# Optimization experiments

Hardware: AMD Instinct MI355X
Metric: run time of the kernel (lower is better)

Reference implementation:

```python
import jax, jax.numpy as jnp
import numpy as np

THRESHOLD = 0.5

def setup_inputs() -> dict:
    key = jax.random.key(0)
    ks = jax.random.split(key, 7)
    dim, hidden = 1024, 4096
    x = jax.random.normal(ks[0], (4, 4096, dim), dtype=jnp.float32)
    # router: Linear(dim, 1)
    W_r = jax.random.normal(ks[1], (dim, 1), dtype=jnp.float32) / np.sqrt(dim)
    b_r = jnp.zeros((1,), dtype=jnp.float32)
    # MLP: Linear(dim, hidden) -> ReLU -> Linear(hidden, dim)
    W1 = jax.random.normal(ks[2], (dim, hidden), dtype=jnp.float32) / np.sqrt(dim)
    b1 = jnp.zeros((hidden,), dtype=jnp.float32)
    W2 = jax.random.normal(ks[3], (hidden, dim), dtype=jnp.float32) / np.sqrt(hidden)
    b2 = jnp.zeros((dim,), dtype=jnp.float32)
    return {"x": x, "W_r": W_r, "b_r": b_r, "W1": W1, "b1": b1, "W2": W2, "b2": b2}

def reference(x, W_r, b_r, W1, b1, W2, b2):
    # router logits per token: [B, S]
    logits = (jnp.einsum('bsd,do->bso', x, W_r) + b_r)[..., 0]
    probs = jax.nn.sigmoid(logits)
    mask = probs > THRESHOLD  # [B, S] bool
    # dense equivalent of gather-MLP-scatter: compute MLP everywhere, select per token
    h = jax.nn.relu(jnp.einsum('bsd,dh->bsh', x, W1) + b1)
    processed = jnp.einsum('bsh,hd->bsd', h, W2) + b2
    output = jnp.where(mask[..., None], processed, x)
    frac = jnp.mean(mask.astype(jnp.float32))
    return (output, frac)
```

## Files before the change

### kernel.cpp

```cpp
#include <hip/hip_runtime.h>
#include <hip/hip_bf16.h>

#define TOKENS 16384
#define DIM 1024
#define HID 4096

typedef __attribute__((ext_vector_type(8))) short short8;
typedef __attribute__((ext_vector_type(4))) float f32x4;

__device__ __forceinline__ unsigned short f2bf(float f) {
  union { float f; unsigned int u; } v; v.f = f;
  unsigned int r = v.u + 0x7fffu + ((v.u >> 16) & 1u);
  return (unsigned short)(r >> 16);
}

__device__ __forceinline__ void async16(const void* g, void* lds) {
  __builtin_amdgcn_global_load_lds((const __attribute__((address_space(1))) void*)g,
                                   (__attribute__((address_space(3))) void*)lds, 16, 0, 0);
}

__global__ __launch_bounds__(256) void router_kernel(
    const float* __restrict__ x, const float* __restrict__ Wr, const float* __restrict__ br,
    float* __restrict__ out, unsigned short* __restrict__ xb,
    int* __restrict__ idx, int* __restrict__ counter)
{
  __shared__ unsigned char selLds[16];
  int wid = threadIdx.x >> 6, lane = threadIdx.x & 63;
  const float4* wr4 = (const float4*)Wr;
  float4 w[4];
#pragma unroll
  for (int j = 0; j < 4; ++j) w[j] = wr4[lane + 64 * j];
  float b0 = br[0];

#pragma unroll
  for (int t = 0; t < 4; ++t) {
    int token = blockIdx.x * 16 + wid * 4 + t;
    const float4* xr = (const float4*)(x + (size_t)token * DIM);
    float4 v[4];
#pragma unroll
    for (int j = 0; j < 4; ++j) v[j] = xr[lane + 64 * j];
    double s = 0.0;
#pragma unroll
    for (int j = 0; j < 4; ++j)
      s += (double)v[j].x * w[j].x + (double)v[j].y * w[j].y +
           (double)v[j].z * w[j].z + (double)v[j].w * w[j].w;
#pragma unroll
    for (int off = 32; off > 0; off >>= 1) s += __shfl_xor(s, off);
    bool sel = ((float)s + b0) > 0.0f;
    if (sel) {
      ushort4* xbr = (ushort4*)(xb + (size_t)token * DIM);
#pragma unroll
      for (int j = 0; j < 4; ++j) {
        ushort4 u;
        u.x = f2bf(v[j].x); u.y = f2bf(v[j].y); u.z = f2bf(v[j].z); u.w = f2bf(v[j].w);
        xbr[lane + 64 * j] = u;
      }
    } else {
      float4* outr = (float4*)(out + (size_t)token * DIM);
#pragma unroll
      for (int j = 0; j < 4; ++j) outr[lane + 64 * j] = v[j];
    }
    if (lane == 0) selLds[wid * 4 + t] = sel ? 1 : 0;
  }
  __syncthreads();
  if (threadIdx.x == 0) {
    int cnt = 0;
#pragma unroll
    for (int i = 0; i < 16; ++i) cnt += selLds[i];
    int p = atomicAdd(counter, cnt);
#pragma unroll
    for (int i = 0; i < 16; ++i)
      if (selLds[i]) idx[p++] = blockIdx.x * 16 + i;
  }
}

__global__ __launch_bounds__(256) void transpose_cast_kernel(
    const float* __restrict__ W, unsigned short* __restrict__ Wt, int R, int C)
{
  __shared__ float tile[32][33];
  int tx = threadIdx.x & 31, ty = threadIdx.x >> 5;
  int c0 = blockIdx.x * 32, r0 = blockIdx.y * 32;
#pragma unroll
  for (int i = 0; i < 32; i += 8)
    tile[ty + i][tx] = W[(size_t)(r0 + ty + i) * C + (c0 + tx)];
  __syncthreads();
#pragma unroll
  for (int i = 0; i < 32; i += 8)
    Wt[(size_t)(c0 + ty + i) * R + (r0 + tx)] = f2bf(tile[tx][ty + i]);
}

__global__ void frac_kernel(const int* __restrict__ counter, float* __restrict__ fr)
{
  fr[0] = (float)(*counter) * (1.0f / (float)TOKENS);
}

template<int N, int K, bool FIRST>
__global__ __launch_bounds__(256) void gemm_kernel(
    const unsigned short* __restrict__ A, const unsigned short* __restrict__ Bt,
    const float* __restrict__ bias, const int* __restrict__ idxp,
    const int* __restrict__ counter,
    unsigned short* __restrict__ Hout, float* __restrict__ Cout)
{
  constexpr int MT = TOKENS / 128;
  constexpr int NWG = (N / 128) * MT;
  constexpr int q = NWG / 8, r = NWG % 8;
  int wg = blockIdx.x;
  int xcd = wg & 7, lin = wg >> 3;
  int swz = (xcd < r ? xcd * (q + 1) : r * (q + 1) + (xcd - r) * q) + lin;
  int colb = swz / MT;
  int rowb = swz % MT;

  int cnt = *counter;
  int row0 = rowb * 128;
  if (row0 >= cnt) return;
  int col0 = colb * 128;

  __shared__ unsigned short As[128 * 32];
  __shared__ unsigned short Bs[128 * 32];
  __shared__ int rowIdx[128];

  int tid = threadIdx.x, wid = tid >> 6, lane = tid & 63;
  if (tid < 128) rowIdx[tid] = idxp[row0 + tid];
  __syncthreads();

  int sRow0 = wid * 16 + (lane >> 2);
  int sRow1 = 64 + sRow0;
  int chunk = (lane & 3) * 8;
  int ar0 = FIRST ? rowIdx[sRow0] : (row0 + sRow0);
  int ar1 = FIRST ? rowIdx[sRow1] : (row0 + sRow1);
  const unsigned short* gA0 = A + (size_t)ar0 * K + chunk;
  const unsigned short* gA1 = A + (size_t)ar1 * K + chunk;
  const unsigned short* gB0 = Bt + (size_t)(col0 + sRow0) * K + chunk;
  const unsigned short* gB1 = Bt + (size_t)(col0 + sRow1) * K + chunk;
  unsigned short* lA0 = As + (size_t)(wid * 16) * 32;
  unsigned short* lA1 = As + (size_t)(64 + wid * 16) * 32;
  unsigned short* lB0 = Bs + (size_t)(wid * 16) * 32;
  unsigned short* lB1 = Bs + (size_t)(64 + wid * 16) * 32;

  f32x4 acc[4][4];
#pragma unroll
  for (int i = 0; i < 4; ++i)
#pragma unroll
    for (int j = 0; j < 4; ++j) acc[i][j] = (f32x4){0.f, 0.f, 0.f, 0.f};

  int wr = (wid >> 1) * 64, wc = (wid & 1) * 64;
  int frow = lane & 15, khalf = lane >> 4;

  for (int k0 = 0; k0 < K; k0 += 32) {
    async16(gA0 + k0, lA0);
    async16(gA1 + k0, lA1);
    async16(gB0 + k0, lB0);
    async16(gB1 + k0, lB1);
    __syncthreads();
    short8 af[4], bfr[4];
#pragma unroll
    for (int mi = 0; mi < 4; ++mi)
      af[mi] = *(const short8*)&As[(size_t)(wr + mi * 16 + frow) * 32 + khalf * 8];
#pragma unroll
    for (int ni = 0; ni < 4; ++ni)
      bfr[ni] = *(const short8*)&Bs[(size_t)(wc + ni * 16 + frow) * 32 + khalf * 8];
#pragma unroll
    for (int mi = 0; mi < 4; ++mi)
#pragma unroll
      for (int ni = 0; ni < 4; ++ni)
        acc[mi][ni] = __builtin_amdgcn_mfma_f32_16x16x32_bf16(af[mi], bfr[ni], acc[mi][ni], 0, 0, 0);
    __syncthreads();
  }

  int cl = lane & 15, rq = lane >> 4;
#pragma unroll
  for (int mi = 0; mi < 4; ++mi) {
#pragma unroll
    for (int ni = 0; ni < 4; ++ni) {
      int col = col0 + wc + ni * 16 + cl;
      float bv = bias[col];
#pragma unroll
      for (int r2 = 0; r2 < 4; ++r2) {
        int rloc = wr + mi * 16 + rq * 4 + r2;
        int grow = row0 + rloc;
        float val = acc[mi][ni][r2] + bv;
        if (FIRST) {
          val = val > 0.f ? val : 0.f;
          Hout[(size_t)grow * N + col] = f2bf(val);
        } else if (grow < cnt) {
          int tok = rowIdx[rloc];
          Cout[(size_t)tok * DIM + col] = val;
        }
      }
    }
  }
}

extern "C" void kernel_launch(void* const* d_in, const int* in_sizes, int n_in,
                              void* d_out, int out_size, void* d_ws, size_t ws_size,
                              hipStream_t stream)
{
  const float* x  = (const float*)d_in[0];
  const float* Wr = (const float*)d_in[1];
  const float* br = (const float*)d_in[2];
  const float* W1 = (const float*)d_in[3];
  const float* b1 = (const float*)d_in[4];
  const float* W2 = (const float*)d_in[5];
  const float* b2 = (const float*)d_in[6];
  float* out = (float*)d_out;

  char* ws = (char*)d_ws;
  int* counter        = (int*)ws;
  int* idx            = (int*)(ws + 256);
  unsigned short* xb  = (unsigned short*)(ws + (1ull  << 20));
  unsigned short* W1T = (unsigned short*)(ws + (34ull << 20));
  unsigned short* W2T = (unsigned short*)(ws + (44ull << 20));
  unsigned short* h   = (unsigned short*)(ws + (54ull << 20));

  hipMemsetAsync(ws, 0, 256 + TOKENS * 4, stream);

  router_kernel<<<TOKENS / 16, 256, 0, stream>>>(x, Wr, br, out, xb, idx, counter);
  transpose_cast_kernel<<<dim3(HID / 32, DIM / 32), 256, 0, stream>>>(W1, W1T, DIM, HID);
  transpose_cast_kernel<<<dim3(DIM / 32, HID / 32), 256, 0, stream>>>(W2, W2T, HID, DIM);
  frac_kernel<<<1, 1, 0, stream>>>(counter, out + (size_t)TOKENS * DIM);

  gemm_kernel<HID, DIM, true><<<(HID / 128) * (TOKENS / 128), 256, 0, stream>>>(
      xb, W1T, b1, idx, counter, h, nullptr);
  gemm_kernel<DIM, HID, false><<<(DIM / 128) * (TOKENS / 128), 256, 0, stream>>>(
      h, W2T, b2, idx, counter, nullptr, out);
}
```

Before: 383.7 us.

## Double-buffer LDS tiles in GEMM and remap workgroups to rows per XCD

Adds a two-stage LDS ping-pong to the GEMM so the async global-to-LDS loads for the next K-step are issued before the MFMA work on the current step. This removes one barrier per iteration and aims to overlap memory latency with compute. It also replaces the contiguous-chunk XCD swizzle with a mapping where consecutive row blocks are spread across XCDs and each XCD walks the column tiles of a row block. The mapping changes L2 reuse patterns, and the extra buffer doubles the LDS footprint, which may reduce occupancy.

```diff
diff --git a/kernel.cpp b/kernel.cpp
--- a/kernel.cpp
+++ b/kernel.cpp
@@ -101,22 +101,19 @@
     const int* __restrict__ counter,
     unsigned short* __restrict__ Hout, float* __restrict__ Cout)
 {
-  constexpr int MT = TOKENS / 128;
-  constexpr int NWG = (N / 128) * MT;
-  constexpr int q = NWG / 8, r = NWG % 8;
-  int wg = blockIdx.x;
-  int xcd = wg & 7, lin = wg >> 3;
-  int swz = (xcd < r ? xcd * (q + 1) : r * (q + 1) + (xcd - r) * q) + lin;
-  int colb = swz / MT;
-  int rowb = swz % MT;
+  constexpr int NT = N / 128;
+  constexpr int KSTEPS = K / 32;
+  int xcd = blockIdx.x & 7, lin = blockIdx.x >> 3;
+  int rowb = (lin / NT) * 8 + xcd;
+  int colb = lin % NT;
 
   int cnt = *counter;
   int row0 = rowb * 128;
   if (row0 >= cnt) return;
   int col0 = colb * 128;
 
-  __shared__ unsigned short As[128 * 32];
-  __shared__ unsigned short Bs[128 * 32];
+  __shared__ unsigned short As[2][128 * 32];
+  __shared__ unsigned short Bs[2][128 * 32];
   __shared__ int rowIdx[128];
 
   int tid = threadIdx.x, wid = tid >> 6, lane = tid & 63;
@@ -132,10 +129,20 @@
   const unsigned short* gA1 = A + (size_t)ar1 * K + chunk;
   const unsigned short* gB0 = Bt + (size_t)(col0 + sRow0) * K + chunk;
   const unsigned short* gB1 = Bt + (size_t)(col0 + sRow1) * K + chunk;
-  unsigned short* lA0 = As + (size_t)(wid * 16) * 32;
-  unsigned short* lA1 = As + (size_t)(64 + wid * 16) * 32;
-  unsigned short* lB0 = Bs + (size_t)(wid * 16) * 32;
-  unsigned short* lB1 = Bs + (size_t)(64 + wid * 16) * 32;
+  unsigned short* lA0 = &As[0][(size_t)(wid * 16) * 32];
+  unsigned short* lA1 = &As[0][(size_t)(64 + wid * 16) * 32];
+  unsigned short* lB0 = &Bs[0][(size_t)(wid * 16) * 32];
+  unsigned short* lB1 = &Bs[0][(size_t)(64 + wid * 16) * 32];
+
+#define STAGE(t, b)                                  \
+  {                                                  \
+    int kk = (t) * 32;                               \
+    int bo = (b) * 128 * 32;                         \
+    async16(gA0 + kk, lA0 + bo);                     \
+    async16(gA1 + kk, lA1 + bo);                     \
+    async16(gB0 + kk, lB0 + bo);                     \
+    async16(gB1 + kk, lB1 + bo);                     \
+  }
 
   f32x4 acc[4][4];
 #pragma unroll
@@ -146,26 +153,28 @@
   int wr = (wid >> 1) * 64, wc = (wid & 1) * 64;
   int frow = lane & 15, khalf = lane >> 4;
 
-  for (int k0 = 0; k0 < K; k0 += 32) {
-    async16(gA0 + k0, lA0);
-    async16(gA1 + k0, lA1);
-    async16(gB0 + k0, lB0);
-    async16(gB1 + k0, lB1);
-    __syncthreads();
+  STAGE(0, 0);
+  __syncthreads();
+
+  int cur = 0;
+  for (int t = 0; t < KSTEPS; ++t) {
+    if (t + 1 < KSTEPS) STAGE(t + 1, cur ^ 1);
     short8 af[4], bfr[4];
 #pragma unroll
     for (int mi = 0; mi < 4; ++mi)
-      af[mi] = *(const short8*)&As[(size_t)(wr + mi * 16 + frow) * 32 + khalf * 8];
+      af[mi] = *(const short8*)&As[cur][(size_t)(wr + mi * 16 + frow) * 32 + khalf * 8];
 #pragma unroll
     for (int ni = 0; ni < 4; ++ni)
-      bfr[ni] = *(const short8*)&Bs[(size_t)(wc + ni * 16 + frow) * 32 + khalf * 8];
+      bfr[ni] = *(const short8*)&Bs[cur][(size_t)(wc + ni * 16 + frow) * 32 + khalf * 8];
 #pragma unroll
     for (int mi = 0; mi < 4; ++mi)
 #pragma unroll
       for (int ni = 0; ni < 4; ++ni)
         acc[mi][ni] = __builtin_amdgcn_mfma_f32_16x16x32_bf16(af[mi], bfr[ni], acc[mi][ni], 0, 0, 0);
     __syncthreads();
-  }
+    cur ^= 1;
+  }
+#undef STAGE
 
   int cl = lane & 15, rq = lane >> 4;
 #pragma unroll
```

New measurement: 383.9 us. About the same (+0.1%).
